# Kernel optimization log

Hardware: AMD Instinct MI355X
Metric: run time of the kernel (lower is better)

## Reference

```python
import jax, jax.numpy as jnp
import numpy as np

N_EMBD = 1024
N_HEAD = 16


def setup_inputs() -> dict:
    key = jax.random.key(0)
    k1, k2, k3, k4, k5 = jax.random.split(key, 5)
    B, T, C = 4, 2048, N_EMBD
    s = 1.0 / np.sqrt(C)
    x = jax.random.normal(k1, (B, T, C), dtype=jnp.float32)
    w_weight = jax.random.normal(k2, (3 * C, C), dtype=jnp.float32) * s
    w_bias = jax.random.normal(k3, (3 * C,), dtype=jnp.float32) * s
    proj_weight = jax.random.normal(k4, (C, C), dtype=jnp.float32) * s
    proj_bias = jax.random.normal(k5, (C,), dtype=jnp.float32) * s
    return {"x": x, "w_weight": w_weight, "w_bias": w_bias,
            "proj_weight": proj_weight, "proj_bias": proj_bias}


def reference(x, w_weight, w_bias, proj_weight, proj_bias):
    B, T, C = x.shape
    nh = N_HEAD
    hs = C // nh
    # fused QKV projection (torch Linear: x @ W^T + b)
    wei = jnp.einsum('btc,oc->bto', x, w_weight) + w_bias
    k, q, v = jnp.split(wei, 3, axis=-1)  # note: chunk order is k, q, v
    # [B, T, nh, hs] -> [B, nh, T, hs]
    key_ = k.reshape(B, T, nh, hs).transpose(0, 2, 1, 3)
    query = q.reshape(B, T, nh, hs).transpose(0, 2, 1, 3)
    value = v.reshape(B, T, nh, hs).transpose(0, 2, 1, 3)
    scale = hs ** (-0.5)
    weight = jnp.einsum('bhqd,bhkd->bhqk', query, key_) * scale
    weight = jax.nn.softmax(weight, axis=-1)
    out = jnp.einsum('bhqk,bhkd->bhqd', weight, value)  # [B, nh, T, hs]
    # Faithful to source bug: transpose(1,2) is discarded; view is taken on
    # the (B, nh, T, hs) layout directly.
    out = out.reshape(B, T, C)
    out = jnp.einsum('btc,oc->bto', out, proj_weight) + proj_bias
    return out
```

## Files before the change

### kernel.cpp

```cpp
#include <hip/hip_runtime.h>
#include <hip/hip_bf16.h>


typedef __attribute__((ext_vector_type(8)))  short bf16x8;
typedef __attribute__((ext_vector_type(4)))  float f32x4;
typedef __attribute__((ext_vector_type(16))) float f32x16;
typedef __attribute__((ext_vector_type(2)))  unsigned u32x2;

typedef __attribute__((address_space(3))) unsigned lds_u32_t;
typedef __attribute__((address_space(1))) unsigned glb_u32_t;

__device__ __forceinline__ void async_cp16(const short* g, short* l) {
    __builtin_amdgcn_global_load_lds((glb_u32_t*)g, (lds_u32_t*)l, 16, 0, 0);
}

__device__ __forceinline__ float exp2fast(float x) {
    return __builtin_amdgcn_exp2f(x);
}

__device__ __forceinline__ short f2bf(float f) {
    union { float f; unsigned u; } v; v.f = f;
    unsigned r = v.u + 0x7fffu + ((v.u >> 16) & 1u);
    return (short)(r >> 16);
}

__device__ __forceinline__ unsigned cvt_pk_bf16(float lo, float hi) {
    unsigned r;
    asm("v_cvt_pk_bf16_f32 %0, %1, %2" : "=v"(r) : "v"(lo), "v"(hi));
    return r;
}

__global__ __launch_bounds__(256) void cvt_kernel(const float4* __restrict__ in,
                                                  short4* __restrict__ out, int n4) {
    int i = blockIdx.x * 256 + threadIdx.x;
    if (i < n4) {
        float4 v = in[i];
        short4 o;
        o.x = f2bf(v.x); o.y = f2bf(v.y); o.z = f2bf(v.z); o.w = f2bf(v.w);
        out[i] = o;
    }
}

template<int EPI>
__global__ __launch_bounds__(256) void gemm_bf16(
    const short* __restrict__ A, const short* __restrict__ W,
    const float* __restrict__ bias, float* __restrict__ outF,
    short* __restrict__ kout, short* __restrict__ qout, short* __restrict__ vtout,
    int M, int N, int K)
{
    __shared__ short lA[128 * 64];
    __shared__ short lB[128 * 64];
    const int tid  = threadIdx.x;
    const int lane = tid & 63;
    const int wave = tid >> 6;
    const int wM = (wave >> 1) * 64;
    const int wN = (wave & 1) * 64;
    const int l15 = lane & 15, l4 = lane >> 4;
    const int rowBase = blockIdx.y * 128;
    const int colBase = blockIdx.x * 128;

    f32x4 acc[4][4] = {};

    for (int k0 = 0; k0 < K; k0 += 64) {
        #pragma unroll
        for (int i = 0; i < 4; ++i) {
            int eo = (i * 256 + tid) * 8;
            int r  = eo >> 6;
            int c  = eo & 63;
            async_cp16(A + (size_t)(rowBase + r) * K + k0 + c, lA + eo);
            async_cp16(W + (size_t)(colBase + r) * K + k0 + c, lB + eo);
        }
        __syncthreads();
        #pragma unroll
        for (int kt = 0; kt < 2; ++kt) {
            bf16x8 af[4], bfr[4];
            #pragma unroll
            for (int mt = 0; mt < 4; ++mt)
                af[mt] = *(const bf16x8*)(lA + (wM + mt * 16 + l15) * 64 + kt * 32 + l4 * 8);
            #pragma unroll
            for (int nt = 0; nt < 4; ++nt)
                bfr[nt] = *(const bf16x8*)(lB + (wN + nt * 16 + l15) * 64 + kt * 32 + l4 * 8);
            #pragma unroll
            for (int mt = 0; mt < 4; ++mt)
                #pragma unroll
                for (int nt = 0; nt < 4; ++nt)
                    acc[mt][nt] = __builtin_amdgcn_mfma_f32_16x16x32_bf16(
                        af[mt], bfr[nt], acc[mt][nt], 0, 0, 0);
        }
        __syncthreads();
    }

    #pragma unroll
    for (int mt = 0; mt < 4; ++mt) {
        #pragma unroll
        for (int nt = 0; nt < 4; ++nt) {
            const int n  = colBase + wN + nt * 16 + l15;
            const int mb = rowBase + wM + mt * 16 + l4 * 4;
            const float bv = bias[n];
            #pragma unroll
            for (int r = 0; r < 4; ++r) {
                const int m = mb + r;
                float val = acc[mt][nt][r] + bv;
                if (EPI == 0) {
                    int b = m >> 11, t = m & 2047;
                    int j = n >> 10, hd = n & 1023;
                    int h = hd >> 6, d = hd & 63;
                    size_t base = ((size_t)(b * 16 + h) * 2048 + t) * 64 + d;
                    if (j == 0)      kout[base] = f2bf(val);
                    else if (j == 1) qout[base] = f2bf(val * 0.180336879f);
                    else             vtout[((size_t)(b * 16 + h) * 64 + d) * 2048 + t] = f2bf(val);
                } else {
                    outF[(size_t)m * N + n] = val;
                }
            }
        }
    }
}

__global__ __launch_bounds__(256) void attn_kernel(
    const short* __restrict__ Q, const short* __restrict__ Km,
    const short* __restrict__ Vt, short* __restrict__ O)
{
    __shared__ short kbuf[2][64 * 64];
    __shared__ short vbuf[2][64 * 64];

    const int tid  = threadIdx.x;
    const int lane = tid & 63;
    const int wave = tid >> 6;
    const int l31 = lane & 31;
    const int l1  = lane >> 5;

    const int b     = blockIdx.x;
    const int xcd   = b & 7;
    const int inner = b >> 3;
    const int bx    = inner & 15;
    const int bh    = xcd * 8 + (inner >> 4);
    const int q0    = bx * 128 + wave * 32;

    const short* Qh = Q  + (size_t)bh * 2048 * 64;
    const short* Kh = Km + (size_t)bh * 2048 * 64;
    const short* Vh = Vt + (size_t)bh * 64 * 2048;

    const int i8 = lane >> 3, i7 = lane & 7;
    const int srcCol = 8 * (i7 ^ i8);
    const int rsw    = (l31 & 7) << 3;

    auto STAGE = [&](int kv, int buf) {
        if (wave < 2) {
            #pragma unroll
            for (int c = 0; c < 4; ++c) {
                int j = wave * 4 + c;
                async_cp16(Kh + (size_t)(kv + 8 * j + i8) * 64 + srcCol,
                           &kbuf[buf][j * 512 + lane * 8]);
            }
        } else {
            #pragma unroll
            for (int c = 0; c < 4; ++c) {
                int j = (wave - 2) * 4 + c;
                async_cp16(Vh + (size_t)(8 * j + i8) * 2048 + kv + srcCol,
                           &vbuf[buf][j * 512 + lane * 8]);
            }
        }
    };

    bf16x8 qf[4];
    #pragma unroll
    for (int s = 0; s < 4; ++s)
        qf[s] = *(const bf16x8*)(Qh + (size_t)(q0 + l31) * 64 + s * 16 + l1 * 8);

    f32x16 o[2] = {};
    float l_run = 0.f;

    STAGE(0, 0);
    __syncthreads();

    int cur = 0;
    for (int it = 0; it < 32; ++it) {
        if (it < 31) STAGE((it + 1) * 64, cur ^ 1);

        f32x16 s2[2] = {};
        #pragma unroll
        for (int t = 0; t < 2; ++t) {
            #pragma unroll
            for (int s = 0; s < 4; ++s) {
                bf16x8 kf = *(const bf16x8*)(
                    &kbuf[cur][(t * 32 + l31) * 64 + ((s * 16 + l1 * 8) ^ rsw)]);
                s2[t] = __builtin_amdgcn_mfma_f32_32x32x16_bf16(kf, qf[s], s2[t], 0, 0, 0);
            }
        }

        float ps0 = 0.f, ps1 = 0.f, ps2 = 0.f, ps3 = 0.f;
        #pragma unroll
        for (int t = 0; t < 2; ++t)
            #pragma unroll
            for (int i = 0; i < 16; ++i) {
                float p = exp2fast(s2[t][i]);
                s2[t][i] = p;
                if ((i & 3) == 0) ps0 += p;
                else if ((i & 3) == 1) ps1 += p;
                else if ((i & 3) == 2) ps2 += p;
                else ps3 += p;
            }
        float ps = (ps0 + ps1) + (ps2 + ps3);
        ps += __shfl_xor(ps, 32);
        l_run += ps;

        bf16x8 pa[4];
        #pragma unroll
        for (int t = 0; t < 2; ++t) {
            #pragma unroll
            for (int sl = 0; sl < 2; ++sl) {
                unsigned A0 = cvt_pk_bf16(s2[t][8 * sl + 0], s2[t][8 * sl + 1]);
                unsigned A1 = cvt_pk_bf16(s2[t][8 * sl + 2], s2[t][8 * sl + 3]);
                unsigned B0 = cvt_pk_bf16(s2[t][8 * sl + 4], s2[t][8 * sl + 5]);
                unsigned B1 = cvt_pk_bf16(s2[t][8 * sl + 6], s2[t][8 * sl + 7]);
                u32x2 ra = __builtin_amdgcn_permlane32_swap(A0, B0, false, false);
                u32x2 rb = __builtin_amdgcn_permlane32_swap(A1, B1, false, false);
                union { unsigned u[4]; bf16x8 v; } w;
                w.u[0] = ra.x;
                w.u[1] = rb.x;
                w.u[2] = ra.y;
                w.u[3] = rb.y;
                pa[2 * t + sl] = w.v;
            }
        }

        #pragma unroll
        for (int s = 0; s < 4; ++s)
            #pragma unroll
            for (int dt = 0; dt < 2; ++dt) {
                bf16x8 vf = *(const bf16x8*)(
                    &vbuf[cur][(dt * 32 + l31) * 64 + ((s * 16 + l1 * 8) ^ rsw)]);
                o[dt] = __builtin_amdgcn_mfma_f32_32x32x16_bf16(pa[s], vf, o[dt], 0, 0, 0);
            }

        __syncthreads();
        cur ^= 1;
    }

    float invl = 1.f / l_run;
    #pragma unroll
    for (int g = 0; g < 4; ++g)
        #pragma unroll
        for (int rr = 0; rr < 4; ++rr) {
            float c = __shfl(invl, rr + 8 * g + 4 * l1);
            int qrow = q0 + rr + 8 * g + 4 * l1;
            size_t base = ((size_t)bh * 2048 + qrow) * 64 + l31;
            O[base]      = f2bf(o[0][g * 4 + rr] * c);
            O[base + 32] = f2bf(o[1][g * 4 + rr] * c);
        }
}

extern "C" void kernel_launch(void* const* d_in, const int* in_sizes, int n_in,
                              void* d_out, int out_size, void* d_ws, size_t ws_size,
                              hipStream_t stream) {
    const float* x  = (const float*)d_in[0];
    const float* ww = (const float*)d_in[1];
    const float* wb = (const float*)d_in[2];
    const float* pwt = (const float*)d_in[3];
    const float* pb  = (const float*)d_in[4];
    float* out = (float*)d_out;

    short* ws  = (short*)d_ws;
    short* xb  = ws;
    short* wwb = xb  + 8192 * 1024;
    short* pwb = wwb + 3072 * 1024;
    short* qb  = pwb + 1024 * 1024;
    short* kb  = qb  + 64 * 2048 * 64;
    short* vtb = kb  + 64 * 2048 * 64;
    short* ob  = vtb + 64 * 2048 * 64;

    cvt_kernel<<<2097152 / 256, 256, 0, stream>>>((const float4*)x,  (short4*)xb,  2097152);
    cvt_kernel<<< 786432 / 256, 256, 0, stream>>>((const float4*)ww, (short4*)wwb,  786432);
    cvt_kernel<<< 262144 / 256, 256, 0, stream>>>((const float4*)pwt,(short4*)pwb,  262144);

    gemm_bf16<0><<<dim3(24, 64), 256, 0, stream>>>(
        xb, wwb, wb, nullptr, kb, qb, vtb, 8192, 3072, 1024);

    attn_kernel<<<1024, 256, 0, stream>>>(qb, kb, vtb, ob);

    gemm_bf16<1><<<dim3(8, 64), 256, 0, stream>>>(
        ob, pwb, pb, out, nullptr, nullptr, nullptr, 8192, 1024, 1024);
}
```

Baseline: 238.9 us.

## Double-buffer GEMM LDS tiles and XOR-swizzle layout to avoid bank conflicts

The bf16 GEMM kernel now keeps two LDS buffers and issues the async global-to-LDS copies for the next K tile before the MFMA work on the current one, so load latency overlaps with compute. It also XOR-swizzles the 16-byte column chunks by row when storing into LDS and applies the same swizzle on reads, to cut LDS bank conflicts on fragment loads. LDS use doubles to 64KB per block, which may lower occupancy. The loop waits on only one barrier per iteration, which depends on the barrier also waiting for the outstanding async loads.

```diff
diff --git a/kernel.cpp b/kernel.cpp
--- a/kernel.cpp
+++ b/kernel.cpp
@@ -48,38 +48,51 @@
     short* __restrict__ kout, short* __restrict__ qout, short* __restrict__ vtout,
     int M, int N, int K)
 {
-    __shared__ short lA[128 * 64];
-    __shared__ short lB[128 * 64];
+    __shared__ short lA[2][128 * 64];
+    __shared__ short lB[2][128 * 64];
     const int tid  = threadIdx.x;
     const int lane = tid & 63;
     const int wave = tid >> 6;
     const int wM = (wave >> 1) * 64;
     const int wN = (wave & 1) * 64;
     const int l15 = lane & 15, l4 = lane >> 4;
+    const int rsw = (lane & 7) << 3;
     const int rowBase = blockIdx.y * 128;
     const int colBase = blockIdx.x * 128;
 
+    auto STAGE = [&](int t, int buf) {
+        const int k0 = t * 64;
+        #pragma unroll
+        for (int i = 0; i < 4; ++i) {
+            int idx = i * 256 + tid;
+            int r   = idx >> 3;
+            int cp  = ((idx & 7) ^ (r & 7)) * 8;
+            int eo  = idx * 8;
+            async_cp16(A + (size_t)(rowBase + r) * K + k0 + cp, &lA[buf][eo]);
+            async_cp16(W + (size_t)(colBase + r) * K + k0 + cp, &lB[buf][eo]);
+        }
+    };
+
     f32x4 acc[4][4] = {};
-
-    for (int k0 = 0; k0 < K; k0 += 64) {
-        #pragma unroll
-        for (int i = 0; i < 4; ++i) {
-            int eo = (i * 256 + tid) * 8;
-            int r  = eo >> 6;
-            int c  = eo & 63;
-            async_cp16(A + (size_t)(rowBase + r) * K + k0 + c, lA + eo);
-            async_cp16(W + (size_t)(colBase + r) * K + k0 + c, lB + eo);
-        }
-        __syncthreads();
+    const int NT = K >> 6;
+
+    STAGE(0, 0);
+    __syncthreads();
+
+    int cur = 0;
+    for (int t = 0; t < NT; ++t) {
+        if (t + 1 < NT) STAGE(t + 1, cur ^ 1);
         #pragma unroll
         for (int kt = 0; kt < 2; ++kt) {
             bf16x8 af[4], bfr[4];
             #pragma unroll
             for (int mt = 0; mt < 4; ++mt)
-                af[mt] = *(const bf16x8*)(lA + (wM + mt * 16 + l15) * 64 + kt * 32 + l4 * 8);
+                af[mt] = *(const bf16x8*)(
+                    &lA[cur][(wM + mt * 16 + l15) * 64 + ((kt * 32 + l4 * 8) ^ rsw)]);
             #pragma unroll
             for (int nt = 0; nt < 4; ++nt)
-                bfr[nt] = *(const bf16x8*)(lB + (wN + nt * 16 + l15) * 64 + kt * 32 + l4 * 8);
+                bfr[nt] = *(const bf16x8*)(
+                    &lB[cur][(wN + nt * 16 + l15) * 64 + ((kt * 32 + l4 * 8) ^ rsw)]);
             #pragma unroll
             for (int mt = 0; mt < 4; ++mt)
                 #pragma unroll
@@ -88,6 +101,7 @@
                         af[mt], bfr[nt], acc[mt][nt], 0, 0, 0);
         }
         __syncthreads();
+        cur ^= 1;
     }
 
     #pragma unroll
```

Result: faster. 222.1 us (-7.1%).
